# Performance work log

Measured on AMD Instinct MI355X. Metric: run time of the kernel, lower is better.

The kernel has to match this reference:

```python
import jax, jax.numpy as jnp
import numpy as np

B, T, C, H = 16, 512, 256, 8
HS_T = C // H   # temporal head size = 32
HS_S = T // H   # spatial head size = 64
EPS = 1e-6


def _ln(x, w, b):
    m = x.mean(-1, keepdims=True)
    v = ((x - m) ** 2).mean(-1, keepdims=True)
    return (x - m) / jnp.sqrt(v + EPS) * w + b


def setup_inputs() -> dict:
    key = jax.random.key(0)
    ks = jax.random.split(key, 16)
    rn = lambda k, s, scale: jax.random.normal(k, s, dtype=jnp.float32) * scale
    inp = {
        "x_T": rn(ks[0], (B, T, C), 1.0),
        "x_S": rn(ks[1], (B, C, T), 1.0),
        # temporal attention: per-head q/k/v projections, stacked [H, hs, C]
        "Wq_t": rn(ks[2], (H, HS_T, C), C ** -0.5),
        "Wk_t": rn(ks[3], (H, HS_T, C), C ** -0.5),
        "Wv_t": rn(ks[4], (H, HS_T, C), C ** -0.5),
        "Wo": rn(ks[5], (C, C), C ** -0.5),
        # spatial attention: per-head q/k over the time axis, stacked [H, hs_s, T]
        "Wq_s": rn(ks[6], (H, HS_S, T), T ** -0.5),
        "Wk_s": rn(ks[7], (H, HS_S, T), T ** -0.5),
        # feed-forward blocks (expansion_factor=4)
        "ff1_w1": rn(ks[8], (4 * C, C), C ** -0.5),
        "ff1_b1": jnp.zeros((4 * C,), jnp.float32),
        "ff1_w2": rn(ks[9], (C, 4 * C), (4 * C) ** -0.5),
        "ff1_b2": jnp.zeros((C,), jnp.float32),
        "ff2_w1": rn(ks[10], (4 * C, C), C ** -0.5),
        "ff2_b1": jnp.zeros((4 * C,), jnp.float32),
        "ff2_w2": rn(ks[11], (C, 4 * C), (4 * C) ** -0.5),
        "ff2_b2": jnp.zeros((C,), jnp.float32),
        # layernorm affine params
        "t_ln1_w": jnp.ones((C,), jnp.float32), "t_ln1_b": jnp.zeros((C,), jnp.float32),
        "t_ln2_w": jnp.ones((C,), jnp.float32), "t_ln2_b": jnp.zeros((C,), jnp.float32),
        "s_ln1_w": jnp.ones((T,), jnp.float32), "s_ln1_b": jnp.zeros((T,), jnp.float32),
        "fus_ln_w": jnp.ones((C,), jnp.float32), "fus_ln_b": jnp.zeros((C,), jnp.float32),
    }
    return inp


def reference(x_T, x_S, Wq_t, Wk_t, Wv_t, Wo, Wq_s, Wk_s,
              ff1_w1, ff1_b1, ff1_w2, ff1_b2, ff2_w1, ff2_b1, ff2_w2, ff2_b2,
              t_ln1_w, t_ln1_b, t_ln2_w, t_ln2_b, s_ln1_w, s_ln1_b,
              fus_ln_w, fus_ln_b):
    # ---- temporal (causal) multi-head attention ----
    h = _ln(x_T, t_ln1_w, t_ln1_b)                         # [B,T,C]
    q = jnp.einsum('btc,hdc->bhtd', h, Wq_t)
    k = jnp.einsum('btc,hdc->bhtd', h, Wk_t)
    v = jnp.einsum('btc,hdc->bhtd', h, Wv_t)
    scores = jnp.einsum('bhtd,bhsd->bhts', q, k) / jnp.sqrt(jnp.float32(HS_T))
    causal = jnp.tril(jnp.ones((T, T), dtype=bool))
    scores = jnp.where(causal, scores, -jnp.inf)
    att = jax.nn.softmax(scores, axis=-1)
    o = jnp.einsum('bhts,bhsd->bhtd', att, v)              # [B,H,T,hs]
    o = o.transpose(0, 2, 1, 3).reshape(B, T, C)           # concat heads
    attn_out = o @ Wo.T
    x = x_T + attn_out
    # FFN 1
    h2 = _ln(x, t_ln2_w, t_ln2_b)
    f = jax.nn.relu(h2 @ ff1_w1.T + ff1_b1) @ ff1_w2.T + ff1_b2
    temporal_out = x + f                                   # [B,T,C]
    # ---- spatial (non-causal) attention over neurons ----
    hs = _ln(x_S, s_ln1_w, s_ln1_b)                        # [B,C,T]
    qs = jnp.einsum('bct,hdt->bhcd', hs, Wq_s)
    ks = jnp.einsum('bct,hdt->bhcd', hs, Wk_s)
    sc = jnp.einsum('bhcd,bhed->bhce', qs, ks) / jnp.sqrt(jnp.float32(HS_S))
    spatial_weights = jax.nn.softmax(sc, axis=-1).mean(axis=1)   # [B,C,C], mean over heads
    # ---- fusion ----
    fused = jnp.einsum('bce,bte->btc', spatial_weights, temporal_out)
    x2 = temporal_out + fused
    h3 = _ln(x2, fus_ln_w, fus_ln_b)
    f2 = jax.nn.relu(h3 @ ff2_w1.T + ff2_b1) @ ff2_w2.T + ff2_b2
    out = x2 + f2
    return out, spatial_weights
```

## Files before the change

### kernel.cpp

```cpp
#include <hip/hip_runtime.h>
#include <hip/hip_bf16.h>

typedef __hip_bfloat16 bf16;
typedef __attribute__((ext_vector_type(8))) short short8;
typedef __attribute__((ext_vector_type(4))) float f32x4;

#define F_BIAS 1
#define F_RELU 2
#define F_RES  4

__device__ __forceinline__ void st_out(float* p, float v){ *p = v; }
__device__ __forceinline__ void st_out(bf16* p, float v){ *p = __float2bfloat16(v); }
__device__ __forceinline__ short f2bs(float f){
  bf16 h = __float2bfloat16(f);
  return *reinterpret_cast<short*>(&h);
}

__device__ __forceinline__ void gl_lds16(const void* g, void* l){
  __builtin_amdgcn_global_load_lds(
      (const __attribute__((address_space(1))) void*)g,
      (__attribute__((address_space(3))) void*)l, 16, 0, 0);
}

__device__ __forceinline__ void lgkm_barrier(){
  asm volatile("s_waitcnt lgkmcnt(0)" ::: "memory");
  __builtin_amdgcn_s_barrier();
}

struct ProArgs {
  const float* wsrc[10];
  bf16* wdst[10];
  const float *xT, *xS, *tl1w, *tl1b, *sl1w, *sl1b;
  bf16 *hT, *hS;
};

template<int RL>
__device__ __forceinline__ void wave_ln(bf16* __restrict__ dst,
    const float* __restrict__ src, const float* __restrict__ w,
    const float* __restrict__ bvec, int row){
  int lane = threadIdx.x & 63;
  const float* s = src + (size_t)row*RL;
  float4 v0 = *(const float4*)(s + lane*4);
  float4 v1 = {0.f,0.f,0.f,0.f};
  float sum = v0.x+v0.y+v0.z+v0.w;
  float sq  = v0.x*v0.x+v0.y*v0.y+v0.z*v0.z+v0.w*v0.w;
  if (RL == 512){
    v1 = *(const float4*)(s + 256 + lane*4);
    sum += v1.x+v1.y+v1.z+v1.w;
    sq  += v1.x*v1.x+v1.y*v1.y+v1.z*v1.z+v1.w*v1.w;
  }
  #pragma unroll
  for (int off=32; off; off>>=1){
    sum += __shfl_xor(sum, off, 64);
    sq  += __shfl_xor(sq , off, 64);
  }
  const float inv = 1.0f/(float)RL;
  float mean = sum*inv;
  float rstd = rsqrtf(sq*inv - mean*mean + 1e-6f);
  float4 w0 = *(const float4*)(w + lane*4);
  float4 b0 = *(const float4*)(bvec + lane*4);
  bf16* d = dst + (size_t)row*RL;
  short4 o;
  o.x = f2bs((v0.x-mean)*rstd*w0.x + b0.x);
  o.y = f2bs((v0.y-mean)*rstd*w0.y + b0.y);
  o.z = f2bs((v0.z-mean)*rstd*w0.z + b0.z);
  o.w = f2bs((v0.w-mean)*rstd*w0.w + b0.w);
  *(short4*)((short*)d + lane*4) = o;
  if (RL == 512){
    float4 w1 = *(const float4*)(w + 256 + lane*4);
    float4 b1 = *(const float4*)(bvec + 256 + lane*4);
    short4 o1;
    o1.x = f2bs((v1.x-mean)*rstd*w1.x + b1.x);
    o1.y = f2bs((v1.y-mean)*rstd*w1.y + b1.y);
    o1.z = f2bs((v1.z-mean)*rstd*w1.z + b1.z);
    o1.w = f2bs((v1.w-mean)*rstd*w1.w + b1.w);
    *(short4*)((short*)d + 256 + lane*4) = o1;
  }
}

__global__ __launch_bounds__(256) void prologue(ProArgs a){
  int blk = blockIdx.x;
  int wid = threadIdx.x >> 6;
  if (blk < 1792){
    int v = blk*256 + threadIdx.x;
    int e = v*4;
    int seg = (e>=65536)+(e>=131072)+(e>=196608)+(e>=262144)+(e>=524288)
            + (e>=786432)+(e>=1048576)+(e>=1310720)+(e>=1572864);
    const int starts[10] = {0,65536,131072,196608,262144,524288,786432,
                            1048576,1310720,1572864};
    int off = e - starts[seg];
    float4 f = *(const float4*)(a.wsrc[seg] + off);
    short4 o;
    o.x = f2bs(f.x); o.y = f2bs(f.y); o.z = f2bs(f.z); o.w = f2bs(f.w);
    *(short4*)((short*)a.wdst[seg] + off) = o;
  } else if (blk < 1792 + 2048){
    wave_ln<256>(a.hT, a.xT, a.tl1w, a.tl1b, (blk-1792)*4 + wid);
  } else {
    wave_ln<512>(a.hS, a.xS, a.sl1w, a.sl1b, (blk-3840)*4 + wid);
  }
}

template<int BM, int BN, int BK>
__device__ __forceinline__ void gemm_body(
    short* __restrict__ AsB, short* __restrict__ BsB,
    const bf16* __restrict__ A, const bf16* __restrict__ B,
    float* __restrict__ outF, bf16* __restrict__ outB,
    const float* __restrict__ bias, const float* __restrict__ resid,
    int K, int lda, int ldb, int ldc, int flags, int m0, int n0){
  int tid = threadIdx.x;
  int w = tid>>6, lane = tid&63, quad = lane>>4, l16 = lane&15;
  constexpr int MF  = BM/32;
  constexpr int NF  = BN/32;
  constexpr int CPR = BK/8;
  constexpr int CA  = BM*CPR/256;
  constexpr int CB  = BN*CPR/256;
  int wm = (w>>1)*(BM/2), wn = (w&1)*(BN/2);
  f32x4 acc[MF][NF];
  #pragma unroll
  for (int r=0;r<MF;r++)
    #pragma unroll
    for (int j=0;j<NF;j++)
      acc[r][j] = (f32x4){0.f,0.f,0.f,0.f};

  auto stage = [&](int k0, int half){
    short* as = AsB + half*(BM*BK);
    short* bs = BsB + half*(BN*BK);
    #pragma unroll
    for (int c=0;c<CA;c++){
      int ch = tid + c*256;
      int row = ch / CPR, p = ch % CPR;
      gl_lds16(A + (size_t)(m0+row)*lda + k0 + ((p ^ (row&(CPR-1)))*8),
               &as[row*BK + p*8]);
    }
    #pragma unroll
    for (int c=0;c<CB;c++){
      int ch = tid + c*256;
      int row = ch / CPR, p = ch % CPR;
      gl_lds16(B + (size_t)(n0+row)*ldb + k0 + ((p ^ (row&(CPR-1)))*8),
               &bs[row*BK + p*8]);
    }
  };

  stage(0, 0);
  int nk = K / BK;
  for (int t = 0; t < nk; ++t){
    __syncthreads();
    if (t+1 < nk) stage((t+1)*BK, (t+1)&1);
    const short* as = AsB + (t&1)*(BM*BK);
    const short* bs = BsB + (t&1)*(BN*BK);
    #pragma unroll
    for (int ks=0; ks<BK/32; ++ks){
      short8 af[MF], bfr[NF];
      #pragma unroll
      for (int r=0;r<MF;r++){
        int rr = wm + r*16 + l16;
        af[r] = *(short8*)&as[rr*BK + (((ks*4+quad) ^ (rr&(CPR-1)))*8)];
      }
      #pragma unroll
      for (int j=0;j<NF;j++){
        int rr = wn + j*16 + l16;
        bfr[j] = *(short8*)&bs[rr*BK + (((ks*4+quad) ^ (rr&(CPR-1)))*8)];
      }
      #pragma unroll
      for (int r=0;r<MF;r++)
        #pragma unroll
        for (int j=0;j<NF;j++)
          acc[r][j] = __builtin_amdgcn_mfma_f32_16x16x32_bf16(af[r], bfr[j], acc[r][j], 0,0,0);
    }
  }
  #pragma unroll
  for (int r=0;r<MF;r++){
    int mb = m0 + wm + r*16 + quad*4;
    #pragma unroll
    for (int j=0;j<NF;j++){
      int n = n0 + wn + j*16 + l16;
      float bv = (flags & F_BIAS) ? bias[n] : 0.0f;
      #pragma unroll
      for (int e=0;e<4;e++){
        float v = acc[r][j][e] + bv;
        if (flags & F_RELU) v = fmaxf(v, 0.0f);
        long long idx = (long long)(mb+e)*ldc + n;
        if (flags & F_RES) v += resid[idx];
        if (outF) outF[idx] = v;
        if (outB) st_out(outB + idx, v);
      }
    }
  }
}

template<int BM, int BN, int BK>
__global__ __launch_bounds__(256) void gemm_mfma(
    const bf16* __restrict__ A, const bf16* __restrict__ B,
    float* __restrict__ outF, bf16* __restrict__ outB,
    const float* __restrict__ bias, const float* __restrict__ resid,
    int K, int lda, int ldb, int ldc, int flags){
  __shared__ __align__(16) short As[2*BM*BK];
  __shared__ __align__(16) short Bs[2*BN*BK];
  gemm_body<BM,BN,BK>(As,Bs,A,B,outF,outB,bias,resid,K,lda,ldb,ldc,flags,
                      blockIdx.x*BM, blockIdx.y*BN);
}

struct GArgs {
  const bf16 *A, *B;
  float* outF; bf16* outB;
  const float *bias, *resid;
  int K, lda, ldb, ldc, flags, ty;
};
__global__ __launch_bounds__(256) void gemm_dual(GArgs g0, GArgs g1, int n0){
  __shared__ __align__(16) short As[2*64*64];
  __shared__ __align__(16) short Bs[2*128*64];
  int id = blockIdx.x;
  bool first = id < n0;
  const GArgs& g = first ? g0 : g1;
  int t = first ? id : id - n0;
  int bx = t / g.ty, by = t - bx*g.ty;
  gemm_body<64,128,64>(As, Bs, g.A, g.B, g.outF, g.outB, g.bias, g.resid,
                       g.K, g.lda, g.ldb, g.ldc, g.flags, bx*64, by*128);
}

__global__ __launch_bounds__(512) void gemm_ln(
    const bf16* __restrict__ A, const bf16* __restrict__ B,
    float* __restrict__ outF, bf16* __restrict__ outLN,
    const float* __restrict__ resid,
    const float* __restrict__ lnw, const float* __restrict__ lnb,
    int K, int lda, int ldb, int flags,
    long long sA, long long sB, long long sO, long long sR){
  int bz = blockIdx.z;
  A += (size_t)bz*sA;
  B += (size_t)bz*sB;
  long long obase = (long long)bz*sO;
  __shared__ __align__(16) short As[2*32*64];
  __shared__ __align__(16) short Bs[2*256*64];
  __shared__ float redS[4][32], redQ[4][32];
  int tid = threadIdx.x;
  int m0 = blockIdx.x*32;
  int w = tid>>6, lane = tid&63, quad = lane>>4, l16 = lane&15;
  int wm = (w>>2)*16;
  int wn = (w&3)*64;
  f32x4 acc[4];
  #pragma unroll
  for (int j=0;j<4;j++) acc[j] = (f32x4){0.f,0.f,0.f,0.f};

  auto stage = [&](int k0, int half){
    short* as = As + half*(32*64);
    short* bs = Bs + half*(256*64);
    if (tid < 256){
      int row = tid >> 3, p = tid & 7;
      gl_lds16(A + (size_t)(m0+row)*lda + k0 + ((p ^ (row&7))*8),
               &as[row*64 + p*8]);
    }
    #pragma unroll
    for (int c=0;c<4;c++){
      int ch = tid + c*512;
      int row = ch >> 3, p = ch & 7;
      gl_lds16(B + (size_t)row*ldb + k0 + ((p ^ (row&7))*8),
               &bs[row*64 + p*8]);
    }
  };

  stage(0, 0);
  int nk = K / 64;
  for (int t = 0; t < nk; ++t){
    __syncthreads();
    if (t+1 < nk) stage((t+1)*64, (t+1)&1);
    const short* as = As + (t&1)*(32*64);
    const short* bs = Bs + (t&1)*(256*64);
    #pragma unroll
    for (int ks=0; ks<2; ++ks){
      int rr = wm + l16;
      short8 af = *(short8*)&as[rr*64 + (((ks*4+quad) ^ (rr&7))*8)];
      #pragma unroll
      for (int j=0;j<4;j++){
        int rb = wn + j*16 + l16;
        short8 bfr = *(short8*)&bs[rb*64 + (((ks*4+quad) ^ (rb&7))*8)];
        acc[j] = __builtin_amdgcn_mfma_f32_16x16x32_bf16(af, bfr, acc[j], 0,0,0);
      }
    }
  }
  #pragma unroll
  for (int e=0;e<4;e++){
    int row = wm + quad*4 + e;
    float s = 0.f, q2 = 0.f;
    #pragma unroll
    for (int j=0;j<4;j++){
      float v = acc[j][e];
      if (flags & F_RES)
        v += resid[(long long)bz*sR + (long long)(m0+row)*256 + wn + j*16 + l16];
      acc[j][e] = v;
      s += v; q2 += v*v;
    }
    #pragma unroll
    for (int off=1; off<16; off<<=1){
      s  += __shfl_xor(s , off, 16);
      q2 += __shfl_xor(q2, off, 16);
    }
    if (l16==0){ redS[w&3][row] = s; redQ[w&3][row] = q2; }
  }
  __syncthreads();
  #pragma unroll
  for (int e=0;e<4;e++){
    int row = wm + quad*4 + e;
    float tot = redS[0][row] + redS[1][row] + redS[2][row] + redS[3][row];
    float tq  = redQ[0][row] + redQ[1][row] + redQ[2][row] + redQ[3][row];
    float mean = tot * (1.0f/256.0f);
    float var  = tq * (1.0f/256.0f) - mean*mean;
    float rstd = rsqrtf(var + 1e-6f);
    #pragma unroll
    for (int j=0;j<4;j++){
      int col = wn + j*16 + l16;
      float v = acc[j][e];
      long long idx = obase + (long long)(m0+row)*256 + col;
      if (outF) outF[idx] = v;
      outLN[idx] = __float2bfloat16((v-mean)*rstd*lnw[col] + lnb[col]);
    }
  }
}

__device__ __forceinline__ int fsw(int row){ return (row>>1)&3; }
__global__ __launch_bounds__(256) void flash_mfma(
    const bf16* __restrict__ qkv, bf16* __restrict__ o){
  int qt = (int)gridDim.x - 1 - (int)blockIdx.x;
  int h = blockIdx.y, b = blockIdx.z;
  int tid = threadIdx.x;
  int w = tid>>6, lane = tid&63, quad = lane>>4, l16 = lane&15;
  __shared__ __align__(16) bf16 Qs[64*32];
  __shared__ __align__(16) bf16 Ks[2][64*32];
  __shared__ __align__(16) bf16 Vt[2][32*72];
  __shared__ __align__(16) bf16 Ps[64*72];
  const bf16* base = qkv + (size_t)b*512*768;
  int t0 = qt*64;
  int srow = tid>>2, spos = tid&3;
  gl_lds16(base + (size_t)(t0+srow)*768 + h*32 + ((spos ^ fsw(srow))*8),
           &Qs[srow*32 + spos*8]);
  {
    const bf16* rp = base + (size_t)srow*768 + h*32;
    gl_lds16(rp + 256 + ((spos ^ fsw(srow))*8), &Ks[0][srow*32 + spos*8]);
    short8 v = *(const short8*)(rp + 512 + spos*8);
    #pragma unroll
    for (int q=0;q<8;q++){
      short tmp = v[q];
      Vt[0][(spos*8+q)*72 + srow] = *(bf16*)&tmp;
    }
  }
  f32x4 accO[2];
  accO[0] = (f32x4){0.f,0.f,0.f,0.f};
  accO[1] = (f32x4){0.f,0.f,0.f,0.f};
  float m_i[4], l_i[4];
  #pragma unroll
  for (int e=0;e<4;e++){ m_i[e] = -3.0e38f; l_i[e] = 0.0f; }
  const float scale = 0.17677669529663687f;
  __syncthreads();
  int rq = w*16 + l16;
  short8 aq = *(short8*)&Qs[rq*32 + ((quad ^ fsw(rq))*8)];

  for (int kt = 0; kt <= qt; ++kt){
    if (kt) __syncthreads();
    int cur = kt&1, nxt = cur^1;
    bool pre = (kt < qt);
    short8 vpre;
    if (pre){
      const bf16* rp = base + (size_t)((kt+1)*64 + srow)*768 + h*32;
      gl_lds16(rp + 256 + ((spos ^ fsw(srow))*8), &Ks[nxt][srow*32 + spos*8]);
      vpre = *(const short8*)(rp + 512 + spos*8);
    }
    f32x4 S[4];
    #pragma unroll
    for (int j2=0;j2<4;j2++){
      int rk = j2*16 + l16;
      short8 bk = *(short8*)&Ks[cur][rk*32 + ((quad ^ fsw(rk))*8)];
      S[j2] = __builtin_amdgcn_mfma_f32_16x16x32_bf16(aq, bk,
                (f32x4){0.f,0.f,0.f,0.f}, 0,0,0);
    }
    bool diag = (kt == qt);
    int s0 = kt*64;
    int qrow_base = t0 + w*16 + quad*4;
    #pragma unroll
    for (int e=0;e<4;e++){
      float sv[4];
      #pragma unroll
      for (int j2=0;j2<4;j2++){
        float x = S[j2][e]*scale;
        if (diag && (s0 + j2*16 + l16 > qrow_base + e)) x = -3.0e38f;
        sv[j2] = x;
      }
      float mx = fmaxf(fmaxf(sv[0],sv[1]), fmaxf(sv[2],sv[3]));
      #pragma unroll
      for (int off=1; off<16; off<<=1) mx = fmaxf(mx, __shfl_xor(mx, off, 64));
      float m_new = fmaxf(m_i[e], mx);
      float alpha = __expf(m_i[e]-m_new);
      float rs = 0.0f;
      #pragma unroll
      for (int j2=0;j2<4;j2++){
        float p = __expf(sv[j2]-m_new);
        rs += p;
        Ps[(w*16+quad*4+e)*72 + j2*16 + l16] = __float2bfloat16(p);
      }
      #pragma unroll
      for (int off=1; off<16; off<<=1) rs += __shfl_xor(rs, off, 64);
      l_i[e] = l_i[e]*alpha + rs;
      m_i[e] = m_new;
      accO[0][e] *= alpha;
      accO[1][e] *= alpha;
    }
    asm volatile("s_waitcnt lgkmcnt(0)" ::: "memory");
    __builtin_amdgcn_sched_barrier(0);
    #pragma unroll
    for (int sh=0; sh<2; ++sh){
      short8 ap = *(short8*)&Ps[(w*16+l16)*72 + sh*32 + quad*8];
      #pragma unroll
      for (int dh=0; dh<2; ++dh){
        short8 bv = *(short8*)&Vt[cur][(dh*16+l16)*72 + sh*32 + quad*8];
        accO[dh] = __builtin_amdgcn_mfma_f32_16x16x32_bf16(ap, bv, accO[dh], 0,0,0);
      }
    }
    if (pre){
      #pragma unroll
      for (int q=0;q<8;q++){
        short tmp = vpre[q];
        Vt[nxt][(spos*8+q)*72 + srow] = *(bf16*)&tmp;
      }
    }
  }
  #pragma unroll
  for (int e=0;e<4;e++){
    float inv = 1.0f/l_i[e];
    int t = t0 + w*16 + quad*4 + e;
    bf16* op = o + ((size_t)(b*512+t))*256 + h*32 + l16;
    op[0]  = __float2bfloat16(accO[0][e]*inv);
    op[16] = __float2bfloat16(accO[1][e]*inv);
  }
}

__global__ __launch_bounds__(256) void spatial_fused(
    const bf16* __restrict__ qk, float* __restrict__ out1,
    bf16* __restrict__ swB){
  int ct = blockIdx.x & 15, b = blockIdx.x >> 4;
  int tid = threadIdx.x;
  int w = tid>>6, lane = tid&63, quad = lane>>4, l16 = lane&15;
  __shared__ __align__(16) bf16 Qall[16*512];
  __shared__ __align__(16) bf16 Ks[2][256*64];
  __shared__ float redM[4][16], redS2[4][16];
  const bf16* qbase = qk + ((size_t)(b*256 + ct*16))*1024;
  #pragma unroll
  for (int c=0;c<4;c++){
    int ch = tid + c*256;
    int row = ch>>6, p = ch&63;
    gl_lds16(qbase + (size_t)row*1024 + ((p ^ (row&7))*8), &Qall[row*512 + p*8]);
  }
  auto stageK = [&](int h, int half){
    bf16* ks = Ks[half];
    #pragma unroll
    for (int c=0;c<8;c++){
      int ch = tid + c*256;
      int e = ch>>3, p = ch&7;
      gl_lds16(qk + ((size_t)(b*256 + e))*1024 + 512 + h*64 + ((p ^ (e&7))*8),
               &ks[e*64 + p*8]);
    }
  };
  stageK(0, 0);
  float fRes[4][4];
  #pragma unroll
  for (int j=0;j<4;j++)
    #pragma unroll
    for (int e=0;e<4;e++) fRes[j][e] = 0.0f;

  for (int h=0; h<8; ++h){
    __syncthreads();
    if (h+1 < 8) stageK(h+1, (h+1)&1);
    const bf16* kcur = Ks[h&1];
    f32x4 acc[4];
    #pragma unroll
    for (int j=0;j<4;j++) acc[j] = (f32x4){0.f,0.f,0.f,0.f};
    #pragma unroll
    for (int ki=0; ki<2; ++ki){
      int g = h*8 + ki*4 + quad;
      short8 aq = *(short8*)&Qall[l16*512 + ((g ^ (l16&7))*8)];
      #pragma unroll
      for (int j=0;j<4;j++){
        int e = w*64 + j*16 + l16;
        short8 bk = *(short8*)&kcur[e*64 + (((ki*4+quad) ^ (e&7))*8)];
        acc[j] = __builtin_amdgcn_mfma_f32_16x16x32_bf16(aq, bk, acc[j], 0,0,0);
      }
    }
    #pragma unroll
    for (int e=0;e<4;e++){
      float m = -3.0e38f;
      #pragma unroll
      for (int j=0;j<4;j++){
        float s = acc[j][e]*0.125f;
        acc[j][e] = s;
        m = fmaxf(m, s);
      }
      #pragma unroll
      for (int off=1; off<16; off<<=1) m = fmaxf(m, __shfl_xor(m, off, 16));
      if (l16==0) redM[w][quad*4+e] = m;
    }
    lgkm_barrier();
    #pragma unroll
    for (int e=0;e<4;e++){
      int r = quad*4+e;
      float m = fmaxf(fmaxf(redM[0][r],redM[1][r]), fmaxf(redM[2][r],redM[3][r]));
      float s = 0.0f;
      #pragma unroll
      for (int j=0;j<4;j++){
        float p = __expf(acc[j][e]-m);
        acc[j][e] = p; s += p;
      }
      #pragma unroll
      for (int off=1; off<16; off<<=1) s += __shfl_xor(s, off, 16);
      if (l16==0) redS2[w][r] = s;
    }
    lgkm_barrier();
    #pragma unroll
    for (int e=0;e<4;e++){
      int r = quad*4+e;
      float tot = redS2[0][r]+redS2[1][r]+redS2[2][r]+redS2[3][r];
      float inv = 0.125f/tot;
      #pragma unroll
      for (int j=0;j<4;j++) fRes[j][e] += acc[j][e]*inv;
    }
  }
  #pragma unroll
  for (int e=0;e<4;e++){
    int c = ct*16 + quad*4 + e;
    size_t rb = ((size_t)b*256 + c)*256;
    #pragma unroll
    for (int j=0;j<4;j++){
      int col = w*64 + j*16 + l16;
      out1[rb+col] = fRes[j][e];
      swB[rb+col]  = __float2bfloat16(fRes[j][e]);
    }
  }
}

extern "C" void kernel_launch(void* const* d_in, const int* in_sizes, int n_in,
                              void* d_out, int out_size, void* d_ws, size_t ws_size,
                              hipStream_t stream){
  (void)in_sizes; (void)n_in; (void)out_size; (void)ws_size;
  const float* x_T  = (const float*)d_in[0];
  const float* x_S  = (const float*)d_in[1];
  const float* Wq_t = (const float*)d_in[2];
  const float* Wk_t = (const float*)d_in[3];
  const float* Wv_t = (const float*)d_in[4];
  const float* Wo   = (const float*)d_in[5];
  const float* Wq_s = (const float*)d_in[6];
  const float* Wk_s = (const float*)d_in[7];
  const float* f1w1 = (const float*)d_in[8];
  const float* f1b1 = (const float*)d_in[9];
  const float* f1w2 = (const float*)d_in[10];
  const float* f1b2 = (const float*)d_in[11];
  const float* f2w1 = (const float*)d_in[12];
  const float* f2b1 = (const float*)d_in[13];
  const float* f2w2 = (const float*)d_in[14];
  const float* f2b2 = (const float*)d_in[15];
  const float* tl1w = (const float*)d_in[16];
  const float* tl1b = (const float*)d_in[17];
  const float* tl2w = (const float*)d_in[18];
  const float* tl2b = (const float*)d_in[19];
  const float* sl1w = (const float*)d_in[20];
  const float* sl1b = (const float*)d_in[21];
  const float* flw  = (const float*)d_in[22];
  const float* flb  = (const float*)d_in[23];

  float* ws = (float*)d_ws;
  size_t off = 0;
  bf16*  Wqkvb  = (bf16*)(ws + off); off += 768*256/2;
  bf16*  Wob    = (bf16*)(ws + off); off += 256*256/2;
  bf16*  f1w1b  = (bf16*)(ws + off); off += 1024*256/2;
  bf16*  f1w2b  = (bf16*)(ws + off); off += 256*1024/2;
  bf16*  f2w1b  = (bf16*)(ws + off); off += 1024*256/2;
  bf16*  f2w2b  = (bf16*)(ws + off); off += 256*1024/2;
  bf16*  WSb    = (bf16*)(ws + off); off += 1024*512/2;
  bf16*  bufHb  = (bf16*)(ws + off); off += (size_t)8192*256/2;
  bf16*  bufHSb = (bf16*)(ws + off); off += (size_t)4096*512/2;
  bf16*  bufQKVb= (bf16*)(ws + off); off += (size_t)8192*768/2;
  bf16*  bufBigB= (bf16*)(ws + off); off += (size_t)8192*1024/2;
  bf16*  bufOb  = (bf16*)(ws + off); off += (size_t)8192*256/2;
  bf16*  bufTOb = (bf16*)(ws + off); off += (size_t)8192*256/2;
  bf16*  swB    = (bf16*)(ws + off); off += (size_t)16*256*256/2;
  bf16*  qkB    = (bf16*)(ws + off); off += (size_t)4096*1024/2;
  float* bufX   = ws + off; off += (size_t)8192*256;
  float* bufTO  = ws + off; off += (size_t)8192*256;
  float* bufX2  = ws + off; off += (size_t)8192*256;

  float* out0 = (float*)d_out;
  float* out1 = out0 + (size_t)16*512*256;

  ProArgs pa;
  pa.wsrc[0]=Wq_t;  pa.wdst[0]=Wqkvb;
  pa.wsrc[1]=Wk_t;  pa.wdst[1]=Wqkvb+65536;
  pa.wsrc[2]=Wv_t;  pa.wdst[2]=Wqkvb+131072;
  pa.wsrc[3]=Wo;    pa.wdst[3]=Wob;
  pa.wsrc[4]=f1w1;  pa.wdst[4]=f1w1b;
  pa.wsrc[5]=f1w2;  pa.wdst[5]=f1w2b;
  pa.wsrc[6]=f2w1;  pa.wdst[6]=f2w1b;
  pa.wsrc[7]=f2w2;  pa.wdst[7]=f2w2b;
  pa.wsrc[8]=Wq_s;  pa.wdst[8]=WSb;
  pa.wsrc[9]=Wk_s;  pa.wdst[9]=WSb+262144;
  pa.xT=x_T; pa.xS=x_S; pa.tl1w=tl1w; pa.tl1b=tl1b;
  pa.sl1w=sl1w; pa.sl1b=sl1b; pa.hT=bufHb; pa.hS=bufHSb;
  prologue<<<4864,256,0,stream>>>(pa);

  GArgs gq, gs;
  gq.A=bufHb;  gq.B=Wqkvb; gq.outF=nullptr; gq.outB=bufQKVb;
  gq.bias=nullptr; gq.resid=nullptr;
  gq.K=256; gq.lda=256; gq.ldb=256; gq.ldc=768; gq.flags=0; gq.ty=6;
  gs.A=bufHSb; gs.B=WSb;   gs.outF=nullptr; gs.outB=qkB;
  gs.bias=nullptr; gs.resid=nullptr;
  gs.K=512; gs.lda=512; gs.ldb=512; gs.ldc=1024; gs.flags=0; gs.ty=8;
  gemm_dual<<<1280,256,0,stream>>>(gq, gs, 768);

  spatial_fused<<<256,256,0,stream>>>(qkB, out1, swB);

  flash_mfma<<<dim3(8,8,16),256,0,stream>>>(bufQKVb, bufOb);
  gemm_ln<<<dim3(256,1,1),512,0,stream>>>(bufOb, Wob, bufX, bufHb,
        x_T, tl2w, tl2b, 256, 256,256, F_RES, 0,0,0,0);
  gemm_mfma<64,128,64><<<dim3(128,8),256,0,stream>>>(bufHb, f1w1b, nullptr, bufBigB,
        f1b1, nullptr, 256, 256,256,1024, F_BIAS|F_RELU);
  gemm_mfma<64,128,64><<<dim3(128,2),256,0,stream>>>(bufBigB, f1w2b, bufTO, bufTOb,
        f1b2, bufX, 1024, 1024,1024,256, F_BIAS|F_RES);
  gemm_ln<<<dim3(16,1,16),512,0,stream>>>(bufTOb, swB, bufX2, bufHb,
        bufTO, flw, flb, 256, 256,256, F_RES,
        131072, 65536, 131072, 131072);
  gemm_mfma<64,128,64><<<dim3(128,8),256,0,stream>>>(bufHb, f2w1b, nullptr, bufBigB,
        f2b1, nullptr, 256, 256,256,1024, F_BIAS|F_RELU);
  gemm_mfma<64,128,64><<<dim3(128,2),256,0,stream>>>(bufBigB, f2w2b, out0, nullptr,
        f2b2, bufX2, 1024, 1024,1024,256, F_BIAS|F_RES);
}
```

Before: 291.4 us.

## Fuse spatial attention and post-attention GEMM chain into one cooperative persistent kernel

Replaces the spatial-attention kernel and the six GEMM/GEMM+LN launches after flash attention with a single cooperative kernel of 256 blocks of 512 threads. Stages are separated by grid.sync() and share one LDS arena. Spatial attention and the FFN GEMMs are re-tiled for 512-thread blocks. The aim is to remove launch gaps and tail effects between many small kernels. In exchange, each grid barrier costs time, the 256-block grid may underfill the GPU for the larger GEMMs, and spatial attention now runs serially after flash attention instead of being independent of it.

```diff
diff --git a/kernel.cpp b/kernel.cpp
--- a/kernel.cpp
+++ b/kernel.cpp
@@ -1,5 +1,8 @@
 #include <hip/hip_runtime.h>
 #include <hip/hip_bf16.h>
+#include <hip/hip_cooperative_groups.h>
+
+namespace cg = cooperative_groups;
 
 typedef __hip_bfloat16 bf16;
 typedef __attribute__((ext_vector_type(8))) short short8;
@@ -188,18 +191,6 @@
   }
 }
 
-template<int BM, int BN, int BK>
-__global__ __launch_bounds__(256) void gemm_mfma(
-    const bf16* __restrict__ A, const bf16* __restrict__ B,
-    float* __restrict__ outF, bf16* __restrict__ outB,
-    const float* __restrict__ bias, const float* __restrict__ resid,
-    int K, int lda, int ldb, int ldc, int flags){
-  __shared__ __align__(16) short As[2*BM*BK];
-  __shared__ __align__(16) short Bs[2*BN*BK];
-  gemm_body<BM,BN,BK>(As,Bs,A,B,outF,outB,bias,resid,K,lda,ldb,ldc,flags,
-                      blockIdx.x*BM, blockIdx.y*BN);
-}
-
 struct GArgs {
   const bf16 *A, *B;
   float* outF; bf16* outB;
@@ -218,22 +209,104 @@
                        g.K, g.lda, g.ldb, g.ldc, g.flags, bx*64, by*128);
 }
 
-__global__ __launch_bounds__(512) void gemm_ln(
+template<int BM, int BN, int BK>
+__device__ __forceinline__ void gemm512_body(
+    short* __restrict__ AsB, short* __restrict__ BsB,
+    const bf16* __restrict__ A, const bf16* __restrict__ B,
+    float* __restrict__ outF, bf16* __restrict__ outB,
+    const float* __restrict__ bias, const float* __restrict__ resid,
+    int K, int lda, int ldb, int ldc, int flags, int m0, int n0){
+  int tid = threadIdx.x;
+  int w = tid>>6, lane = tid&63, quad = lane>>4, l16 = lane&15;
+  constexpr int MF  = BM/32;
+  constexpr int NF  = BN/64;
+  constexpr int CPR = BK/8;
+  constexpr int CA  = BM*CPR/512;
+  constexpr int CB  = BN*CPR/512;
+  int wm = (w>>2)*(BM/2), wn = (w&3)*(BN/4);
+  f32x4 acc[MF][NF];
+  #pragma unroll
+  for (int r=0;r<MF;r++)
+    #pragma unroll
+    for (int j=0;j<NF;j++)
+      acc[r][j] = (f32x4){0.f,0.f,0.f,0.f};
+
+  auto stage = [&](int k0, int half){
+    short* as = AsB + half*(BM*BK);
+    short* bs = BsB + half*(BN*BK);
+    #pragma unroll
+    for (int c=0;c<CA;c++){
+      int ch = tid + c*512;
+      int row = ch / CPR, p = ch % CPR;
+      gl_lds16(A + (size_t)(m0+row)*lda + k0 + ((p ^ (row&(CPR-1)))*8),
+               &as[row*BK + p*8]);
+    }
+    #pragma unroll
+    for (int c=0;c<CB;c++){
+      int ch = tid + c*512;
+      int row = ch / CPR, p = ch % CPR;
+      gl_lds16(B + (size_t)(n0+row)*ldb + k0 + ((p ^ (row&(CPR-1)))*8),
+               &bs[row*BK + p*8]);
+    }
+  };
+
+  stage(0, 0);
+  int nk = K / BK;
+  for (int t = 0; t < nk; ++t){
+    __syncthreads();
+    if (t+1 < nk) stage((t+1)*BK, (t+1)&1);
+    const short* as = AsB + (t&1)*(BM*BK);
+    const short* bs = BsB + (t&1)*(BN*BK);
+    #pragma unroll
+    for (int ks=0; ks<BK/32; ++ks){
+      short8 af[MF], bfr[NF];
+      #pragma unroll
+      for (int r=0;r<MF;r++){
+        int rr = wm + r*16 + l16;
+        af[r] = *(short8*)&as[rr*BK + (((ks*4+quad) ^ (rr&(CPR-1)))*8)];
+      }
+      #pragma unroll
+      for (int j=0;j<NF;j++){
+        int rr = wn + j*16 + l16;
+        bfr[j] = *(short8*)&bs[rr*BK + (((ks*4+quad) ^ (rr&(CPR-1)))*8)];
+      }
+      #pragma unroll
+      for (int r=0;r<MF;r++)
+        #pragma unroll
+        for (int j=0;j<NF;j++)
+          acc[r][j] = __builtin_amdgcn_mfma_f32_16x16x32_bf16(af[r], bfr[j], acc[r][j], 0,0,0);
+    }
+  }
+  #pragma unroll
+  for (int r=0;r<MF;r++){
+    int mb = m0 + wm + r*16 + quad*4;
+    #pragma unroll
+    for (int j=0;j<NF;j++){
+      int n = n0 + wn + j*16 + l16;
+      float bv = (flags & F_BIAS) ? bias[n] : 0.0f;
+      #pragma unroll
+      for (int e=0;e<4;e++){
+        float v = acc[r][j][e] + bv;
+        if (flags & F_RELU) v = fmaxf(v, 0.0f);
+        long long idx = (long long)(mb+e)*ldc + n;
+        if (flags & F_RES) v += resid[idx];
+        if (outF) outF[idx] = v;
+        if (outB) st_out(outB + idx, v);
+      }
+    }
+  }
+}
+
+__device__ void gemm_ln_body(short* arena, float (*redS)[32], float (*redQ)[32],
     const bf16* __restrict__ A, const bf16* __restrict__ B,
     float* __restrict__ outF, bf16* __restrict__ outLN,
     const float* __restrict__ resid,
     const float* __restrict__ lnw, const float* __restrict__ lnb,
-    int K, int lda, int ldb, int flags,
-    long long sA, long long sB, long long sO, long long sR){
-  int bz = blockIdx.z;
-  A += (size_t)bz*sA;
-  B += (size_t)bz*sB;
-  long long obase = (long long)bz*sO;
-  __shared__ __align__(16) short As[2*32*64];
-  __shared__ __align__(16) short Bs[2*256*64];
-  __shared__ float redS[4][32], redQ[4][32];
+    int K, int lda, int ldb, int flags, int m0,
+    long long obase, long long rbase){
+  short* As = arena;
+  short* Bs = arena + 4096;
   int tid = threadIdx.x;
-  int m0 = blockIdx.x*32;
   int w = tid>>6, lane = tid&63, quad = lane>>4, l16 = lane&15;
   int wm = (w>>2)*16;
   int wn = (w&3)*64;
@@ -285,7 +358,7 @@
     for (int j=0;j<4;j++){
       float v = acc[j][e];
       if (flags & F_RES)
-        v += resid[(long long)bz*sR + (long long)(m0+row)*256 + wn + j*16 + l16];
+        v += resid[rbase + (long long)(m0+row)*256 + wn + j*16 + l16];
       acc[j][e] = v;
       s += v; q2 += v*v;
     }
@@ -312,6 +385,107 @@
       long long idx = obase + (long long)(m0+row)*256 + col;
       if (outF) outF[idx] = v;
       outLN[idx] = __float2bfloat16((v-mean)*rstd*lnw[col] + lnb[col]);
+    }
+  }
+}
+
+__device__ void spatial512(short* arena, float (*redM)[32], float (*redS2)[32],
+                           const bf16* __restrict__ qk,
+                           float* __restrict__ out1, bf16* __restrict__ swB,
+                           int ct, int b){
+  bf16* Qall = (bf16*)arena;
+  bf16* KsB  = (bf16*)(arena + 8192);
+  int tid = threadIdx.x;
+  int w = tid>>6, lane = tid&63, quad = lane>>4, l16 = lane&15;
+  const bf16* qbase = qk + ((size_t)(b*256 + ct*16))*1024;
+  #pragma unroll
+  for (int c=0;c<2;c++){
+    int ch = tid + c*512;
+    int row = ch>>6, p = ch&63;
+    gl_lds16(qbase + (size_t)row*1024 + ((p ^ (row&7))*8), &Qall[row*512 + p*8]);
+  }
+  auto stageK = [&](int h, int half){
+    bf16* ks = KsB + half*(256*64);
+    #pragma unroll
+    for (int c=0;c<4;c++){
+      int ch = tid + c*512;
+      int e = ch>>3, p = ch&7;
+      gl_lds16(qk + ((size_t)(b*256 + e))*1024 + 512 + h*64 + ((p ^ (e&7))*8),
+               &ks[e*64 + p*8]);
+    }
+  };
+  stageK(0, 0);
+  float fRes[2][4];
+  #pragma unroll
+  for (int j=0;j<2;j++)
+    #pragma unroll
+    for (int e=0;e<4;e++) fRes[j][e] = 0.0f;
+
+  for (int h=0; h<8; ++h){
+    __syncthreads();
+    if (h+1 < 8) stageK(h+1, (h+1)&1);
+    const bf16* kcur = KsB + (h&1)*(256*64);
+    f32x4 acc[2];
+    acc[0] = (f32x4){0.f,0.f,0.f,0.f};
+    acc[1] = (f32x4){0.f,0.f,0.f,0.f};
+    #pragma unroll
+    for (int ki=0; ki<2; ++ki){
+      int g = h*8 + ki*4 + quad;
+      short8 aq = *(short8*)&Qall[l16*512 + ((g ^ (l16&7))*8)];
+      #pragma unroll
+      for (int j=0;j<2;j++){
+        int e = w*32 + j*16 + l16;
+        short8 bk = *(short8*)&kcur[e*64 + (((ki*4+quad) ^ (e&7))*8)];
+        acc[j] = __builtin_amdgcn_mfma_f32_16x16x32_bf16(aq, bk, acc[j], 0,0,0);
+      }
+    }
+    #pragma unroll
+    for (int e=0;e<4;e++){
+      float s0 = acc[0][e]*0.125f, s1 = acc[1][e]*0.125f;
+      acc[0][e] = s0; acc[1][e] = s1;
+      float m = fmaxf(s0, s1);
+      #pragma unroll
+      for (int off=1; off<16; off<<=1) m = fmaxf(m, __shfl_xor(m, off, 16));
+      if (l16==0) redM[w][quad*4+e] = m;
+    }
+    lgkm_barrier();
+    #pragma unroll
+    for (int e=0;e<4;e++){
+      int r = quad*4+e;
+      float m = redM[0][r];
+      #pragma unroll
+      for (int ww=1; ww<8; ww++) m = fmaxf(m, redM[ww][r]);
+      float s = 0.0f;
+      #pragma unroll
+      for (int j=0;j<2;j++){
+        float p = __expf(acc[j][e]-m);
+        acc[j][e] = p; s += p;
+      }
+      #pragma unroll
+      for (int off=1; off<16; off<<=1) s += __shfl_xor(s, off, 16);
+      if (l16==0) redS2[w][r] = s;
+    }
+    lgkm_barrier();
+    #pragma unroll
+    for (int e=0;e<4;e++){
+      int r = quad*4+e;
+      float tot = 0.0f;
+      #pragma unroll
+      for (int ww=0; ww<8; ww++) tot += redS2[ww][r];
+      float inv = 0.125f/tot;
+      #pragma unroll
+      for (int j=0;j<2;j++) fRes[j][e] += acc[j][e]*inv;
+    }
+  }
+  #pragma unroll
+  for (int e=0;e<4;e++){
+    int c = ct*16 + quad*4 + e;
+    size_t rb = ((size_t)b*256 + c)*256;
+    #pragma unroll
+    for (int j=0;j<2;j++){
+      int col = w*32 + j*16 + l16;
+      out1[rb+col] = fRes[j][e];
+      swB[rb+col]  = __float2bfloat16(fRes[j][e]);
     }
   }
 }
@@ -431,106 +605,64 @@
   }
 }
 
-__global__ __launch_bounds__(256) void spatial_fused(
-    const bf16* __restrict__ qk, float* __restrict__ out1,
-    bf16* __restrict__ swB){
-  int ct = blockIdx.x & 15, b = blockIdx.x >> 4;
-  int tid = threadIdx.x;
-  int w = tid>>6, lane = tid&63, quad = lane>>4, l16 = lane&15;
-  __shared__ __align__(16) bf16 Qall[16*512];
-  __shared__ __align__(16) bf16 Ks[2][256*64];
-  __shared__ float redM[4][16], redS2[4][16];
-  const bf16* qbase = qk + ((size_t)(b*256 + ct*16))*1024;
-  #pragma unroll
-  for (int c=0;c<4;c++){
-    int ch = tid + c*256;
-    int row = ch>>6, p = ch&63;
-    gl_lds16(qbase + (size_t)row*1024 + ((p ^ (row&7))*8), &Qall[row*512 + p*8]);
-  }
-  auto stageK = [&](int h, int half){
-    bf16* ks = Ks[half];
-    #pragma unroll
-    for (int c=0;c<8;c++){
-      int ch = tid + c*256;
-      int e = ch>>3, p = ch&7;
-      gl_lds16(qk + ((size_t)(b*256 + e))*1024 + 512 + h*64 + ((p ^ (e&7))*8),
-               &ks[e*64 + p*8]);
-    }
-  };
-  stageK(0, 0);
-  float fRes[4][4];
-  #pragma unroll
-  for (int j=0;j<4;j++)
-    #pragma unroll
-    for (int e=0;e<4;e++) fRes[j][e] = 0.0f;
-
-  for (int h=0; h<8; ++h){
-    __syncthreads();
-    if (h+1 < 8) stageK(h+1, (h+1)&1);
-    const bf16* kcur = Ks[h&1];
-    f32x4 acc[4];
-    #pragma unroll
-    for (int j=0;j<4;j++) acc[j] = (f32x4){0.f,0.f,0.f,0.f};
-    #pragma unroll
-    for (int ki=0; ki<2; ++ki){
-      int g = h*8 + ki*4 + quad;
-      short8 aq = *(short8*)&Qall[l16*512 + ((g ^ (l16&7))*8)];
-      #pragma unroll
-      for (int j=0;j<4;j++){
-        int e = w*64 + j*16 + l16;
-        short8 bk = *(short8*)&kcur[e*64 + (((ki*4+quad) ^ (e&7))*8)];
-        acc[j] = __builtin_amdgcn_mfma_f32_16x16x32_bf16(aq, bk, acc[j], 0,0,0);
-      }
-    }
-    #pragma unroll
-    for (int e=0;e<4;e++){
-      float m = -3.0e38f;
-      #pragma unroll
-      for (int j=0;j<4;j++){
-        float s = acc[j][e]*0.125f;
-        acc[j][e] = s;
-        m = fmaxf(m, s);
-      }
-      #pragma unroll
-      for (int off=1; off<16; off<<=1) m = fmaxf(m, __shfl_xor(m, off, 16));
-      if (l16==0) redM[w][quad*4+e] = m;
-    }
-    lgkm_barrier();
-    #pragma unroll
-    for (int e=0;e<4;e++){
-      int r = quad*4+e;
-      float m = fmaxf(fmaxf(redM[0][r],redM[1][r]), fmaxf(redM[2][r],redM[3][r]));
-      float s = 0.0f;
-      #pragma unroll
-      for (int j=0;j<4;j++){
-        float p = __expf(acc[j][e]-m);
-        acc[j][e] = p; s += p;
-      }
-      #pragma unroll
-      for (int off=1; off<16; off<<=1) s += __shfl_xor(s, off, 16);
-      if (l16==0) redS2[w][r] = s;
-    }
-    lgkm_barrier();
-    #pragma unroll
-    for (int e=0;e<4;e++){
-      int r = quad*4+e;
-      float tot = redS2[0][r]+redS2[1][r]+redS2[2][r]+redS2[3][r];
-      float inv = 0.125f/tot;
-      #pragma unroll
-      for (int j=0;j<4;j++) fRes[j][e] += acc[j][e]*inv;
-    }
-  }
-  #pragma unroll
-  for (int e=0;e<4;e++){
-    int c = ct*16 + quad*4 + e;
-    size_t rb = ((size_t)b*256 + c)*256;
-    #pragma unroll
-    for (int j=0;j<4;j++){
-      int col = w*64 + j*16 + l16;
-      out1[rb+col] = fRes[j][e];
-      swB[rb+col]  = __float2bfloat16(fRes[j][e]);
-    }
-  }
+struct MegaArgs {
+  const bf16 *qk; float* out1; bf16* swB;
+  const bf16 *bufOb, *Wob; float* bufX; bf16* bufHb; const float* xT;
+  const float *tl2w, *tl2b;
+  const bf16 *f1w1b; bf16* bufBigB; const float* f1b1;
+  const bf16 *f1w2b; float* bufTO; bf16* bufTOb; const float* f1b2;
+  float* bufX2; const float *flw, *flb;
+  const bf16 *f2w1b; const float* f2b1;
+  const bf16 *f2w2b; float* out0; const float* f2b2;
+};
+
+__global__ __launch_bounds__(512) void mega(MegaArgs a){
+  __shared__ __align__(16) short arena[40960];
+  __shared__ float redA[8][32], redB[8][32];
+  cg::grid_group grid = cg::this_grid();
+  int blk = blockIdx.x;
+
+  spatial512(arena, redA, redB, a.qk, a.out1, a.swB, blk & 15, blk >> 4);
+  grid.sync();
+
+  gemm_ln_body(arena, redA, redB, a.bufOb, a.Wob, a.bufX, a.bufHb, a.xT,
+               a.tl2w, a.tl2b, 256, 256, 256, F_RES, blk*32, 0, 0);
+  grid.sync();
+
+  for (int i=0;i<4;i++){
+    int t = blk + i*256;
+    gemm512_body<64,128,64>(arena, arena + 8192, a.bufHb, a.f1w1b,
+        nullptr, a.bufBigB, a.f1b1, nullptr,
+        256, 256, 256, 1024, F_BIAS|F_RELU, (t>>3)*64, (t&7)*128);
+  }
+  grid.sync();
+
+  gemm512_body<64,128,64>(arena, arena + 8192, a.bufBigB, a.f1w2b,
+      a.bufTO, a.bufTOb, a.f1b2, a.bufX,
+      1024, 1024, 1024, 256, F_BIAS|F_RES, (blk>>1)*64, (blk&1)*128);
+  grid.sync();
+
+  {
+    int bz = blk >> 4, bx = blk & 15;
+    gemm_ln_body(arena, redA, redB,
+        a.bufTOb + (size_t)bz*131072, a.swB + (size_t)bz*65536,
+        a.bufX2, a.bufHb, a.bufTO, a.flw, a.flb,
+        256, 256, 256, F_RES, bx*32,
+        (long long)bz*131072, (long long)bz*131072);
+  }
+  grid.sync();
+
+  for (int i=0;i<4;i++){
+    int t = blk + i*256;
+    gemm512_body<64,128,64>(arena, arena + 8192, a.bufHb, a.f2w1b,
+        nullptr, a.bufBigB, a.f2b1, nullptr,
+        256, 256, 256, 1024, F_BIAS|F_RELU, (t>>3)*64, (t&7)*128);
+  }
+  grid.sync();
+
+  gemm512_body<64,128,64>(arena, arena + 8192, a.bufBigB, a.f2w2b,
+      a.out0, (bf16*)nullptr, a.f2b2, a.bufX2,
+      1024, 1024, 1024, 256, F_BIAS|F_RES, (blk>>1)*64, (blk&1)*128);
 }
 
 extern "C" void kernel_launch(void* const* d_in, const int* in_sizes, int n_in,
@@ -610,20 +742,18 @@
   gs.K=512; gs.lda=512; gs.ldb=512; gs.ldc=1024; gs.flags=0; gs.ty=8;
   gemm_dual<<<1280,256,0,stream>>>(gq, gs, 768);
 
-  spatial_fused<<<256,256,0,stream>>>(qkB, out1, swB);
-
   flash_mfma<<<dim3(8,8,16),256,0,stream>>>(bufQKVb, bufOb);
-  gemm_ln<<<dim3(256,1,1),512,0,stream>>>(bufOb, Wob, bufX, bufHb,
-        x_T, tl2w, tl2b, 256, 256,256, F_RES, 0,0,0,0);
-  gemm_mfma<64,128,64><<<dim3(128,8),256,0,stream>>>(bufHb, f1w1b, nullptr, bufBigB,
-        f1b1, nullptr, 256, 256,256,1024, F_BIAS|F_RELU);
-  gemm_mfma<64,128,64><<<dim3(128,2),256,0,stream>>>(bufBigB, f1w2b, bufTO, bufTOb,
-        f1b2, bufX, 1024, 1024,1024,256, F_BIAS|F_RES);
-  gemm_ln<<<dim3(16,1,16),512,0,stream>>>(bufTOb, swB, bufX2, bufHb,
-        bufTO, flw, flb, 256, 256,256, F_RES,
-        131072, 65536, 131072, 131072);
-  gemm_mfma<64,128,64><<<dim3(128,8),256,0,stream>>>(bufHb, f2w1b, nullptr, bufBigB,
-        f2b1, nullptr, 256, 256,256,1024, F_BIAS|F_RELU);
-  gemm_mfma<64,128,64><<<dim3(128,2),256,0,stream>>>(bufBigB, f2w2b, out0, nullptr,
-        f2b2, bufX2, 1024, 1024,1024,256, F_BIAS|F_RES);
-}
+
+  MegaArgs ma;
+  ma.qk=qkB; ma.out1=out1; ma.swB=swB;
+  ma.bufOb=bufOb; ma.Wob=Wob; ma.bufX=bufX; ma.bufHb=bufHb; ma.xT=x_T;
+  ma.tl2w=tl2w; ma.tl2b=tl2b;
+  ma.f1w1b=f1w1b; ma.bufBigB=bufBigB; ma.f1b1=f1b1;
+  ma.f1w2b=f1w2b; ma.bufTO=bufTO; ma.bufTOb=bufTOb; ma.f1b2=f1b2;
+  ma.bufX2=bufX2; ma.flw=flw; ma.flb=flb;
+  ma.f2w1b=f2w1b; ma.f2b1=f2b1;
+  ma.f2w2b=f2w2b; ma.out0=out0; ma.f2b2=f2b2;
+  void* kargs[] = { (void*)&ma };
+  hipLaunchCooperativeKernel((const void*)mega, dim3(256), dim3(512),
+                             kargs, 0, stream);
+}
```

Result: slower. 487.6 us (+67.3%).

## Fuse FFN up and down projections into one kernel with LDS-resident hidden

Applied to the files above, without the earlier changes.

Replaces the two-GEMM feed-forward sequence with a single kernel. Each 512-thread block owns 32 rows: it computes the ReLU hidden layer tile by tile, keeps the full 32x1024 bf16 hidden block in swizzled LDS, then runs the down projection with bias and residual. This removes the global round trip of the 8192x1024 intermediate and one launch per FFN. In exchange, every block re-streams both full weight matrices from L2. The large LDS footprint (about 144KB) allows only one block per CU, which limits latency hiding.

```diff
diff --git a/kernel.cpp b/kernel.cpp
--- a/kernel.cpp
+++ b/kernel.cpp
@@ -188,18 +188,6 @@
   }
 }
 
-template<int BM, int BN, int BK>
-__global__ __launch_bounds__(256) void gemm_mfma(
-    const bf16* __restrict__ A, const bf16* __restrict__ B,
-    float* __restrict__ outF, bf16* __restrict__ outB,
-    const float* __restrict__ bias, const float* __restrict__ resid,
-    int K, int lda, int ldb, int ldc, int flags){
-  __shared__ __align__(16) short As[2*BM*BK];
-  __shared__ __align__(16) short Bs[2*BN*BK];
-  gemm_body<BM,BN,BK>(As,Bs,A,B,outF,outB,bias,resid,K,lda,ldb,ldc,flags,
-                      blockIdx.x*BM, blockIdx.y*BN);
-}
-
 struct GArgs {
   const bf16 *A, *B;
   float* outF; bf16* outB;
@@ -312,6 +300,130 @@
       long long idx = obase + (long long)(m0+row)*256 + col;
       if (outF) outF[idx] = v;
       outLN[idx] = __float2bfloat16((v-mean)*rstd*lnw[col] + lnb[col]);
+    }
+  }
+}
+
+struct FfnArgs {
+  const bf16 *A;
+  const bf16 *W1;
+  const float *B1;
+  const bf16 *W2;
+  const float *B2;
+  const float *resid;
+  float *outF;
+  bf16  *outB;
+};
+
+__global__ __launch_bounds__(512) void ffn(FfnArgs a){
+  __shared__ __align__(16) short Afull[32*256];
+  __shared__ __align__(16) short Hs[32*1024];
+  __shared__ __align__(16) short Bst[2*16384];
+  int tid = threadIdx.x;
+  int w = tid>>6, lane = tid&63, quad = lane>>4, l16 = lane&15;
+  int m0 = blockIdx.x*32;
+  int wm  = (w>>2)*16;
+  int wnA = (w&3)*32;
+  int wnB = (w&3)*64;
+
+  #pragma unroll
+  for (int c=0;c<2;c++){
+    int ch = tid + c*512;
+    int row = ch>>5, p = ch&31;
+    gl_lds16(a.A + (size_t)(m0+row)*256 + ((p ^ row)*8), &Afull[ch*8]);
+  }
+  auto stageA = [&](int i, int half){
+    short* bs = Bst + half*16384;
+    int nc = i>>2, kt = i&3;
+    #pragma unroll
+    for (int c=0;c<2;c++){
+      int ch = tid + c*512;
+      int row = ch>>3, p = ch&7;
+      gl_lds16(a.W1 + (size_t)(nc*128+row)*256 + kt*64 + ((p ^ (row&7))*8),
+               &bs[ch*8]);
+    }
+  };
+  auto stageB = [&](int kt, int half){
+    short* bs = Bst + half*16384;
+    #pragma unroll
+    for (int c=0;c<4;c++){
+      int ch = tid + c*512;
+      int row = ch>>3, p = ch&7;
+      gl_lds16(a.W2 + (size_t)row*1024 + kt*64 + ((p ^ (row&7))*8),
+               &bs[ch*8]);
+    }
+  };
+
+  stageA(0, 0);
+  f32x4 acc[2];
+  for (int i=0; i<32; ++i){
+    __syncthreads();
+    if (i+1 < 32) stageA(i+1, (i+1)&1);
+    const short* bs = Bst + (i&1)*16384;
+    int kt = i&3, nc = i>>2;
+    if (kt==0){
+      acc[0] = (f32x4){0.f,0.f,0.f,0.f};
+      acc[1] = (f32x4){0.f,0.f,0.f,0.f};
+    }
+    #pragma unroll
+    for (int ks=0; ks<2; ++ks){
+      int rr = wm + l16;
+      int kk = kt*8 + ks*4 + quad;
+      short8 af = *(short8*)&Afull[rr*256 + ((kk ^ rr)*8)];
+      #pragma unroll
+      for (int j=0;j<2;j++){
+        int rb = wnA + j*16 + l16;
+        short8 bk = *(short8*)&bs[rb*64 + (((ks*4+quad) ^ (rb&7))*8)];
+        acc[j] = __builtin_amdgcn_mfma_f32_16x16x32_bf16(af, bk, acc[j], 0,0,0);
+      }
+    }
+    if (kt==3){
+      #pragma unroll
+      for (int j=0;j<2;j++)
+        #pragma unroll
+        for (int e=0;e<4;e++){
+          int row = wm + quad*4 + e;
+          int col = nc*128 + wnA + j*16 + l16;
+          float v = fmaxf(acc[j][e] + a.B1[col], 0.0f);
+          int grp = col>>3;
+          Hs[row*1024 + ((grp ^ (row&7))<<3) + (col&7)] = f2bs(v);
+        }
+    }
+  }
+
+  stageB(0, 0);
+  __syncthreads();
+  f32x4 accB[4];
+  #pragma unroll
+  for (int j=0;j<4;j++) accB[j] = (f32x4){0.f,0.f,0.f,0.f};
+  for (int kt=0; kt<16; ++kt){
+    if (kt) __syncthreads();
+    if (kt+1 < 16) stageB(kt+1, (kt+1)&1);
+    const short* bs = Bst + (kt&1)*16384;
+    #pragma unroll
+    for (int ks=0; ks<2; ++ks){
+      int rr = wm + l16;
+      int kk = kt*8 + ks*4 + quad;
+      short8 af = *(short8*)&Hs[rr*1024 + ((kk ^ (rr&7))*8)];
+      #pragma unroll
+      for (int j=0;j<4;j++){
+        int rb = wnB + j*16 + l16;
+        short8 bk = *(short8*)&bs[rb*64 + (((ks*4+quad) ^ (rb&7))*8)];
+        accB[j] = __builtin_amdgcn_mfma_f32_16x16x32_bf16(af, bk, accB[j], 0,0,0);
+      }
+    }
+  }
+  #pragma unroll
+  for (int j=0;j<4;j++){
+    int n = wnB + j*16 + l16;
+    float bv = a.B2[n];
+    #pragma unroll
+    for (int e=0;e<4;e++){
+      int row = m0 + wm + quad*4 + e;
+      long long idx = (long long)row*256 + n;
+      float v = accB[j][e] + bv + a.resid[idx];
+      a.outF[idx] = v;
+      if (a.outB) st_out(a.outB + idx, v);
     }
   }
 }
@@ -574,7 +686,6 @@
   bf16*  bufHb  = (bf16*)(ws + off); off += (size_t)8192*256/2;
   bf16*  bufHSb = (bf16*)(ws + off); off += (size_t)4096*512/2;
   bf16*  bufQKVb= (bf16*)(ws + off); off += (size_t)8192*768/2;
-  bf16*  bufBigB= (bf16*)(ws + off); off += (size_t)8192*1024/2;
   bf16*  bufOb  = (bf16*)(ws + off); off += (size_t)8192*256/2;
   bf16*  bufTOb = (bf16*)(ws + off); off += (size_t)8192*256/2;
   bf16*  swB    = (bf16*)(ws + off); off += (size_t)16*256*256/2;
@@ -615,15 +726,15 @@
   flash_mfma<<<dim3(8,8,16),256,0,stream>>>(bufQKVb, bufOb);
   gemm_ln<<<dim3(256,1,1),512,0,stream>>>(bufOb, Wob, bufX, bufHb,
         x_T, tl2w, tl2b, 256, 256,256, F_RES, 0,0,0,0);
-  gemm_mfma<64,128,64><<<dim3(128,8),256,0,stream>>>(bufHb, f1w1b, nullptr, bufBigB,
-        f1b1, nullptr, 256, 256,256,1024, F_BIAS|F_RELU);
-  gemm_mfma<64,128,64><<<dim3(128,2),256,0,stream>>>(bufBigB, f1w2b, bufTO, bufTOb,
-        f1b2, bufX, 1024, 1024,1024,256, F_BIAS|F_RES);
+  FfnArgs fa1;
+  fa1.A=bufHb; fa1.W1=f1w1b; fa1.B1=f1b1; fa1.W2=f1w2b; fa1.B2=f1b2;
+  fa1.resid=bufX; fa1.outF=bufTO; fa1.outB=bufTOb;
+  ffn<<<256,512,0,stream>>>(fa1);
   gemm_ln<<<dim3(16,1,16),512,0,stream>>>(bufTOb, swB, bufX2, bufHb,
         bufTO, flw, flb, 256, 256,256, F_RES,
         131072, 65536, 131072, 131072);
-  gemm_mfma<64,128,64><<<dim3(128,8),256,0,stream>>>(bufHb, f2w1b, nullptr, bufBigB,
-        f2b1, nullptr, 256, 256,256,1024, F_BIAS|F_RELU);
-  gemm_mfma<64,128,64><<<dim3(128,2),256,0,stream>>>(bufBigB, f2w2b, out0, nullptr,
-        f2b2, bufX2, 1024, 1024,1024,256, F_BIAS|F_RES);
-}
+  FfnArgs fa2;
+  fa2.A=bufHb; fa2.W1=f2w1b; fa2.B1=f2b1; fa2.W2=f2w2b; fa2.B2=f2b2;
+  fa2.resid=bufX2; fa2.outF=out0; fa2.outB=nullptr;
+  ffn<<<256,512,0,stream>>>(fa2);
+}
```

Measured after the change: 294.2 us. No clear change (+1.0%).
